# Performance work log

Hardware: AMD Instinct MI355X
Metric: run time of the kernel (lower is better)

## Reference

```python
import jax, jax.numpy as jnp
import numpy as np

LOG_STD2 = float(np.log(0.001))  # matches nn.init posterior_W_u/v fill, unused: params are random here


def _mvg_layer(x, M, u, v, eps):
    # append ones column (bias trick): [B, in] -> [B, in+1]
    x1 = jnp.concatenate([x, jnp.ones((x.shape[0], 1), x.dtype)], axis=1)
    # W = M + diag(exp(.5u)) @ eps @ diag(exp(.5v))  ==  M + row/col scaled eps
    W = M + jnp.exp(0.5 * u)[:, None] * eps * jnp.exp(0.5 * v)[None, :]
    return x1 @ W


def setup_inputs() -> dict:
    key = jax.random.key(0)
    ks = jax.random.split(key, 17)
    dims = [(2049, 4096), (4097, 4096), (4097, 4096), (4097, 2048)]
    inp = {"x": jax.random.normal(ks[0], (8192, 2048), dtype=jnp.float32)}
    ki = 1
    for i, (fin, fout) in enumerate(dims):
        inp[f"M{i}"] = jax.random.normal(ks[ki], (fin, fout), dtype=jnp.float32) * 0.001; ki += 1
        inp[f"u{i}"] = jax.random.normal(ks[ki], (fin,), dtype=jnp.float32) + LOG_STD2; ki += 1
        inp[f"v{i}"] = jax.random.normal(ks[ki], (fout,), dtype=jnp.float32) + LOG_STD2; ki += 1
        inp[f"eps{i}"] = jax.random.normal(ks[ki], (fin, fout), dtype=jnp.float32); ki += 1
    return inp


def reference(x, M0, u0, v0, eps0, M1, u1, v1, eps1, M2, u2, v2, eps2, M3, u3, v3, eps3):
    h = _mvg_layer(x, M0, u0, v0, eps0)
    h = _mvg_layer(jax.nn.relu(h), M1, u1, v1, eps1)
    h = _mvg_layer(jax.nn.relu(h), M2, u2, v2, eps2)
    h = _mvg_layer(jax.nn.relu(h), M3, u3, v3, eps3)
    return h
```

## Files before the change

kernel.cpp:

```cpp
#include <hip/hip_runtime.h>
#include <cstdint>
#include <cstddef>

typedef __bf16 bf16_t;
typedef __attribute__((ext_vector_type(8))) __bf16 bf16x8;
typedef __attribute__((ext_vector_type(4))) __bf16 bf16x4;
typedef __attribute__((ext_vector_type(4))) float floatx4;

#define SB0 __builtin_amdgcn_sched_barrier(0)
#define LGKM(N)                                          \
  do {                                                   \
    asm volatile("s_waitcnt lgkmcnt(" #N ")" ::: "memory"); \
    SB0;                                                 \
  } while (0)

__device__ __forceinline__ void cp16(const void* g, void* l) {
  __builtin_amdgcn_global_load_lds(
      (const __attribute__((address_space(1))) void*)(uintptr_t)g,
      (__attribute__((address_space(3))) void*)(uintptr_t)l, 16, 0, 0);
}

__device__ __forceinline__ void stage_half(const bf16_t* p, int K, char* dst,
                                           int tid) {
  cp16(p, dst + tid * 16);
  cp16(p + (size_t)128 * K, dst + 8192 + tid * 16);
}

__global__ void cvt_to_bf16(const float4* __restrict__ in,
                            bf16x4* __restrict__ out, int n4) {
  int i = blockIdx.x * 256 + threadIdx.x;
  if (i < n4) {
    float4 f = in[i];
    bf16x4 o;
    o[0] = (bf16_t)f.x; o[1] = (bf16_t)f.y; o[2] = (bf16_t)f.z; o[3] = (bf16_t)f.w;
    out[i] = o;
  }
}

__global__ void prep_wt(const float* __restrict__ M, const float* __restrict__ u,
                        const float* __restrict__ v, const float* __restrict__ eps,
                        bf16_t* __restrict__ Wt, int K, int N) {
  __shared__ float tile[32][33];
  const int nb = blockIdx.x * 32, kb = blockIdx.y * 32;
  const int tx = threadIdx.x, ty = threadIdx.y;
  const float sv = __expf(0.5f * v[nb + tx]);
#pragma unroll
  for (int r = 0; r < 4; ++r) {
    const int k = kb + ty + 8 * r;
    const float su = __expf(0.5f * u[k]);
    const size_t idx = (size_t)k * N + nb + tx;
    tile[ty + 8 * r][tx] = M[idx] + su * eps[idx] * sv;
  }
  __syncthreads();
#pragma unroll
  for (int r = 0; r < 4; ++r) {
    const int n = nb + ty + 8 * r;
    Wt[(size_t)n * K + kb + tx] = (bf16_t)tile[tx][ty + 8 * r];
  }
}

struct BiasArgs {
  const float* M[4];
  const float* u[4];
  const float* v[4];
  const float* e[4];
  float* b[4];
};
__global__ void prep_bias_all(BiasArgs a) {
  const int bid = blockIdx.x;
  int layer, base;
  if (bid < 16) { layer = 0; base = bid; }
  else if (bid < 32) { layer = 1; base = bid - 16; }
  else if (bid < 48) { layer = 2; base = bid - 32; }
  else { layer = 3; base = bid - 48; }
  const int K = (layer == 0) ? 2048 : 4096;
  const int N = (layer == 3) ? 2048 : 4096;
  const int n = base * 256 + threadIdx.x;
  if (n < N) {
    const size_t idx = (size_t)K * N + n;
    a.b[layer][n] = a.M[layer][idx] +
                    __expf(0.5f * a.u[layer][K]) * a.e[layer][idx] *
                        __expf(0.5f * a.v[layer][n]);
  }
}

template <int I0>
__device__ __forceinline__ void mfma_quad(const bf16x8 (&bb)[4], bf16x8 a,
                                          floatx4 (&acc)[8][4]) {
#pragma unroll
  for (int j = 0; j < 4; ++j)
    acc[I0][j] =
        __builtin_amdgcn_mfma_f32_16x16x32_bf16(bb[j], a, acc[I0][j], 0, 0, 0);
}

template <int I0>
__device__ __forceinline__ void phaseA(const char* Ab, const char* Bb,
                                       bf16x8 (&bb)[4], floatx4 (&acc)[8][4]) {
  bf16x8 af0 = *(const bf16x8*)(Ab + (I0 + 0) * 1024);
  bb[0] = *(const bf16x8*)(Bb);
  bb[1] = *(const bf16x8*)(Bb + 1024);
  bb[2] = *(const bf16x8*)(Bb + 2048);
  bb[3] = *(const bf16x8*)(Bb + 3072);
  SB0;
  bf16x8 af1 = *(const bf16x8*)(Ab + (I0 + 1) * 1024);
  SB0;
  bf16x8 af2 = *(const bf16x8*)(Ab + (I0 + 2) * 1024);
  SB0;
  bf16x8 af3 = *(const bf16x8*)(Ab + (I0 + 3) * 1024);
  __builtin_amdgcn_s_setprio(1);
  LGKM(3);
  mfma_quad<I0 + 0>(bb, af0, acc);
  LGKM(2);
  mfma_quad<I0 + 1>(bb, af1, acc);
  LGKM(1);
  mfma_quad<I0 + 2>(bb, af2, acc);
  LGKM(0);
  mfma_quad<I0 + 3>(bb, af3, acc);
  __builtin_amdgcn_s_setprio(0);
}

template <int I0>
__device__ __forceinline__ void phaseB(const char* Ab, const bf16x8 (&bb)[4],
                                       floatx4 (&acc)[8][4]) {
  bf16x8 af0 = *(const bf16x8*)(Ab + (I0 + 0) * 1024);
  SB0;
  bf16x8 af1 = *(const bf16x8*)(Ab + (I0 + 1) * 1024);
  SB0;
  bf16x8 af2 = *(const bf16x8*)(Ab + (I0 + 2) * 1024);
  SB0;
  bf16x8 af3 = *(const bf16x8*)(Ab + (I0 + 3) * 1024);
  __builtin_amdgcn_s_setprio(1);
  LGKM(3);
  mfma_quad<I0 + 0>(bb, af0, acc);
  LGKM(2);
  mfma_quad<I0 + 1>(bb, af1, acc);
  LGKM(1);
  mfma_quad<I0 + 2>(bb, af2, acc);
  LGKM(0);
  mfma_quad<I0 + 3>(bb, af3, acc);
  __builtin_amdgcn_s_setprio(0);
}

template <int CURB>
__device__ __forceinline__ void ktile(int t, int NT, int K,
                                      const bf16_t* gA, const bf16_t* gB,
                                      char* lds, int tid, int aoff0, int boff0,
                                      floatx4 (&acc)[8][4]) {
  constexpr int curO = CURB * 65536;
  constexpr int nxtO = (CURB ^ 1) * 65536;
  bf16x8 bb[4];
  const char* Ab0 = lds + curO + aoff0;
  const char* Ab1 = lds + curO + 16384 + aoff0;
  const char* Bb0 = lds + curO + 32768 + boff0;
  const char* Bb1 = lds + curO + 49152 + boff0;

  if (t + 1 < NT)
    stage_half(gA + (size_t)(t + 1) * 64 + 32, K, lds + nxtO + 16384, tid);
  phaseA<0>(Ab0, Bb0, bb, acc);
  __builtin_amdgcn_s_barrier();
  SB0;

  if (t + 1 < NT)
    stage_half(gB + (size_t)(t + 1) * 64 + 32, K, lds + nxtO + 49152, tid);
  phaseB<4>(Ab0, bb, acc);
  __builtin_amdgcn_s_barrier();
  SB0;

  if (t + 2 < NT)
    stage_half(gA + (size_t)(t + 2) * 64, K, lds + curO, tid);
  phaseA<0>(Ab1, Bb1, bb, acc);
  __builtin_amdgcn_s_barrier();
  SB0;

  if (t + 2 < NT)
    stage_half(gB + (size_t)(t + 2) * 64, K, lds + curO + 32768, tid);
  phaseB<4>(Ab1, bb, acc);
  if (t + 2 < NT) {
    asm volatile("s_waitcnt vmcnt(4)" ::: "memory");
  } else if (t + 1 < NT) {
    asm volatile("s_waitcnt vmcnt(0)" ::: "memory");
  }
  SB0;
  __builtin_amdgcn_s_barrier();
  SB0;
}

template <int EPI>
__global__ __launch_bounds__(512, 2) void gemm256(
    const bf16_t* __restrict__ A, const bf16_t* __restrict__ Bt,
    const float* __restrict__ bias, void* __restrict__ Cout, int N, int K) {
  extern __shared__ char lds[];
  const int tid = threadIdx.x;
  const int lane = tid & 63;
  const int wave = tid >> 6;
  const int wm = (wave >> 2) * 128;
  const int wn = (wave & 3) * 64;
  const int l15 = lane & 15;
  const int kqs = ((lane >> 4) ^ ((lane >> 1) & 3)) << 4;
  const int aoff0 = (wm + l15) * 64 + kqs;
  const int bofB0 = (wn + l15) * 64 + kqs;

  const int gx = gridDim.x;
  int id = blockIdx.y * gx + blockIdx.x;
  const int cpx = (gx * (int)gridDim.y) >> 3;
  id = (id & 7) * cpx + (id >> 3);
  const int bm = (id / gx) * 256;
  const int bn = (id % gx) * 256;

  const int srow = tid >> 2;
  const int ss8 = ((tid & 3) ^ ((tid >> 3) & 3)) * 8;
  const bf16_t* gA = A + (size_t)(bm + srow) * K + ss8;
  const bf16_t* gB = Bt + (size_t)(bn + srow) * K + ss8;

  const int NT = K >> 6;

  floatx4 acc[8][4] = {};

  stage_half(gA, K, lds + 0, tid);
  stage_half(gA + 32, K, lds + 16384, tid);
  stage_half(gB, K, lds + 32768, tid);
  stage_half(gB + 32, K, lds + 49152, tid);
  stage_half(gA + 64, K, lds + 65536, tid);
  stage_half(gB + 64, K, lds + 65536 + 32768, tid);
  asm volatile("s_waitcnt vmcnt(4)" ::: "memory");
  __builtin_amdgcn_s_barrier();
  SB0;

  for (int t = 0; t < NT; t += 2) {
    ktile<0>(t, NT, K, gA, gB, lds, tid, aoff0, bofB0, acc);
    ktile<1>(t + 1, NT, K, gA, gB, lds, tid, aoff0, bofB0, acc);
  }

  const int kq4 = lane >> 4;
  const int row00 = bm + wm + l15;
  const int colq = bn + wn + kq4 * 4;
  float4 b4[4];
#pragma unroll
  for (int j = 0; j < 4; ++j) b4[j] = *(const float4*)&bias[colq + j * 16];
#pragma unroll
  for (int i = 0; i < 8; ++i) {
    const size_t rbase = (size_t)(row00 + i * 16) * N;
#pragma unroll
    for (int j = 0; j < 4; ++j) {
      float x0 = acc[i][j][0] + b4[j].x;
      float x1 = acc[i][j][1] + b4[j].y;
      float x2 = acc[i][j][2] + b4[j].z;
      float x3 = acc[i][j][3] + b4[j].w;
      if (EPI == 0) {
        x0 = fmaxf(x0, 0.f);
        x1 = fmaxf(x1, 0.f);
        x2 = fmaxf(x2, 0.f);
        x3 = fmaxf(x3, 0.f);
        bf16x4 o;
        o[0] = (bf16_t)x0; o[1] = (bf16_t)x1; o[2] = (bf16_t)x2; o[3] = (bf16_t)x3;
        *(bf16x4*)((bf16_t*)Cout + rbase + colq + j * 16) = o;
      } else {
        float4 o = make_float4(x0, x1, x2, x3);
        *(float4*)((float*)Cout + rbase + colq + j * 16) = o;
      }
    }
  }
}

extern "C" void kernel_launch(void* const* d_in, const int* in_sizes, int n_in,
                              void* d_out, int out_size, void* d_ws, size_t ws_size,
                              hipStream_t stream) {
  const float* x = (const float*)d_in[0];
  const float *Mm[4], *uu[4], *vv[4], *ee[4];
  for (int i = 0; i < 4; ++i) {
    Mm[i] = (const float*)d_in[1 + 4 * i];
    uu[i] = (const float*)d_in[2 + 4 * i];
    vv[i] = (const float*)d_in[3 + 4 * i];
    ee[i] = (const float*)d_in[4 + 4 * i];
  }

  char* ws = (char*)d_ws;
  bf16_t* Wt0 = (bf16_t*)ws;
  bf16_t* Wt1 = (bf16_t*)(ws + 16777216);
  bf16_t* Wt2 = (bf16_t*)(ws + 16777216 + 33554432);
  bf16_t* Wt3 = (bf16_t*)(ws + 16777216 + 2u * 33554432);
  char* bptr = ws + 2u * 16777216 + 2u * 33554432;
  float* bias0 = (float*)(bptr);
  float* bias1 = (float*)(bptr + 16384);
  float* bias2 = (float*)(bptr + 32768);
  float* bias3 = (float*)(bptr + 49152);
  char* act = bptr + 65536;
  bf16_t* hA = (bf16_t*)act;
  bf16_t* hB = (bf16_t*)(act + 67108864);
  bf16_t* xb = (bf16_t*)d_out;

  static bool attr_set = false;
  if (!attr_set) {
    (void)hipFuncSetAttribute(reinterpret_cast<const void*>(&gemm256<0>),
                              hipFuncAttributeMaxDynamicSharedMemorySize, 131072);
    (void)hipFuncSetAttribute(reinterpret_cast<const void*>(&gemm256<1>),
                              hipFuncAttributeMaxDynamicSharedMemorySize, 131072);
    attr_set = true;
  }

  cvt_to_bf16<<<16384, 256, 0, stream>>>((const float4*)x, (bf16x4*)xb,
                                         8192 * 2048 / 4);
  prep_wt<<<dim3(4096 / 32, 2048 / 32), dim3(32, 8), 0, stream>>>(
      Mm[0], uu[0], vv[0], ee[0], Wt0, 2048, 4096);
  prep_wt<<<dim3(4096 / 32, 4096 / 32), dim3(32, 8), 0, stream>>>(
      Mm[1], uu[1], vv[1], ee[1], Wt1, 4096, 4096);
  prep_wt<<<dim3(4096 / 32, 4096 / 32), dim3(32, 8), 0, stream>>>(
      Mm[2], uu[2], vv[2], ee[2], Wt2, 4096, 4096);
  prep_wt<<<dim3(2048 / 32, 4096 / 32), dim3(32, 8), 0, stream>>>(
      Mm[3], uu[3], vv[3], ee[3], Wt3, 4096, 2048);
  BiasArgs ba;
  for (int i = 0; i < 4; ++i) {
    ba.M[i] = Mm[i]; ba.u[i] = uu[i]; ba.v[i] = vv[i]; ba.e[i] = ee[i];
  }
  ba.b[0] = bias0; ba.b[1] = bias1; ba.b[2] = bias2; ba.b[3] = bias3;
  prep_bias_all<<<56, 256, 0, stream>>>(ba);

  gemm256<0><<<dim3(16, 32), 512, 131072, stream>>>(xb, Wt0, bias0, hA, 4096, 2048);
  gemm256<0><<<dim3(16, 32), 512, 131072, stream>>>(hA, Wt1, bias1, hB, 4096, 4096);
  gemm256<0><<<dim3(16, 32), 512, 131072, stream>>>(hB, Wt2, bias2, hA, 4096, 4096);
  gemm256<1><<<dim3(8, 32), 512, 131072, stream>>>(hA, Wt3, bias3, d_out, 2048, 4096);
}
```

Baseline: 1.169 ms.

## Switch GEMM to 32x32x16 MFMA and merge prep kernels into one launch

New measurement: 1.268 ms. +8.4%, slower.

```diff
diff --git a/kernel.cpp b/kernel.cpp
--- a/kernel.cpp
+++ b/kernel.cpp
@@ -5,13 +5,13 @@
 typedef __bf16 bf16_t;
 typedef __attribute__((ext_vector_type(8))) __bf16 bf16x8;
 typedef __attribute__((ext_vector_type(4))) __bf16 bf16x4;
-typedef __attribute__((ext_vector_type(4))) float floatx4;
+typedef __attribute__((ext_vector_type(16))) float floatx16;
 
 #define SB0 __builtin_amdgcn_sched_barrier(0)
-#define LGKM(N)                                          \
-  do {                                                   \
+#define LGKM(N)                                             \
+  do {                                                      \
     asm volatile("s_waitcnt lgkmcnt(" #N ")" ::: "memory"); \
-    SB0;                                                 \
+    SB0;                                                    \
   } while (0)
 
 __device__ __forceinline__ void cp16(const void* g, void* l) {
@@ -26,23 +26,63 @@
   cp16(p + (size_t)128 * K, dst + 8192 + tid * 16);
 }
 
-__global__ void cvt_to_bf16(const float4* __restrict__ in,
-                            bf16x4* __restrict__ out, int n4) {
-  int i = blockIdx.x * 256 + threadIdx.x;
-  if (i < n4) {
-    float4 f = in[i];
+struct PrepArgs {
+  const float* x;
+  bf16_t* xb;
+  const float* M[4];
+  const float* u[4];
+  const float* v[4];
+  const float* e[4];
+  bf16_t* Wt[4];
+  float* bias[4];
+};
+
+__global__ __launch_bounds__(256) void prep_all(PrepArgs a) {
+  __shared__ float tile[32][33];
+  const int tx = threadIdx.x, ty = threadIdx.y;
+  const int tid = ty * 32 + tx;
+  int bid = blockIdx.x;
+
+  if (bid < 16384) {
+    const int i = bid * 256 + tid;
+    float4 f = ((const float4*)a.x)[i];
     bf16x4 o;
     o[0] = (bf16_t)f.x; o[1] = (bf16_t)f.y; o[2] = (bf16_t)f.z; o[3] = (bf16_t)f.w;
-    out[i] = o;
-  }
-}
-
-__global__ void prep_wt(const float* __restrict__ M, const float* __restrict__ u,
-                        const float* __restrict__ v, const float* __restrict__ eps,
-                        bf16_t* __restrict__ Wt, int K, int N) {
-  __shared__ float tile[32][33];
-  const int nb = blockIdx.x * 32, kb = blockIdx.y * 32;
-  const int tx = threadIdx.x, ty = threadIdx.y;
+    ((bf16x4*)a.xb)[i] = o;
+    return;
+  }
+  bid -= 16384;
+
+  if (bid >= 49152) {
+    const int b = bid - 49152;
+    int layer, base;
+    if (b < 16) { layer = 0; base = b; }
+    else if (b < 32) { layer = 1; base = b - 16; }
+    else if (b < 48) { layer = 2; base = b - 32; }
+    else { layer = 3; base = b - 48; }
+    const int K = (layer == 0) ? 2048 : 4096;
+    const int N = (layer == 3) ? 2048 : 4096;
+    const int n = base * 256 + tid;
+    if (n < N) {
+      const size_t idx = (size_t)K * N + n;
+      a.bias[layer][n] = a.M[layer][idx] +
+                         __expf(0.5f * a.u[layer][K]) * a.e[layer][idx] *
+                             __expf(0.5f * a.v[layer][n]);
+    }
+    return;
+  }
+
+  int layer, nbx, kby, K, N;
+  if (bid < 8192) { layer = 0; K = 2048; N = 4096; nbx = bid & 127; kby = bid >> 7; }
+  else if (bid < 24576) { layer = 1; K = 4096; N = 4096; int b = bid - 8192; nbx = b & 127; kby = b >> 7; }
+  else if (bid < 40960) { layer = 2; K = 4096; N = 4096; int b = bid - 24576; nbx = b & 127; kby = b >> 7; }
+  else { layer = 3; K = 4096; N = 2048; int b = bid - 40960; nbx = b & 63; kby = b >> 6; }
+  const float* M = a.M[layer];
+  const float* u = a.u[layer];
+  const float* v = a.v[layer];
+  const float* eps = a.e[layer];
+  bf16_t* Wt = a.Wt[layer];
+  const int nb = nbx * 32, kb = kby * 32;
   const float sv = __expf(0.5f * v[nb + tx]);
 #pragma unroll
   for (int r = 0; r < 4; ++r) {
@@ -59,122 +99,69 @@
   }
 }
 
-struct BiasArgs {
-  const float* M[4];
-  const float* u[4];
-  const float* v[4];
-  const float* e[4];
-  float* b[4];
-};
-__global__ void prep_bias_all(BiasArgs a) {
-  const int bid = blockIdx.x;
-  int layer, base;
-  if (bid < 16) { layer = 0; base = bid; }
-  else if (bid < 32) { layer = 1; base = bid - 16; }
-  else if (bid < 48) { layer = 2; base = bid - 32; }
-  else { layer = 3; base = bid - 48; }
-  const int K = (layer == 0) ? 2048 : 4096;
-  const int N = (layer == 3) ? 2048 : 4096;
-  const int n = base * 256 + threadIdx.x;
-  if (n < N) {
-    const size_t idx = (size_t)K * N + n;
-    a.b[layer][n] = a.M[layer][idx] +
-                    __expf(0.5f * a.u[layer][K]) * a.e[layer][idx] *
-                        __expf(0.5f * a.v[layer][n]);
-  }
-}
-
-template <int I0>
-__device__ __forceinline__ void mfma_quad(const bf16x8 (&bb)[4], bf16x8 a,
-                                          floatx4 (&acc)[8][4]) {
-#pragma unroll
-  for (int j = 0; j < 4; ++j)
-    acc[I0][j] =
-        __builtin_amdgcn_mfma_f32_16x16x32_bf16(bb[j], a, acc[I0][j], 0, 0, 0);
-}
-
-template <int I0>
-__device__ __forceinline__ void phaseA(const char* Ab, const char* Bb,
-                                       bf16x8 (&bb)[4], floatx4 (&acc)[8][4]) {
-  bf16x8 af0 = *(const bf16x8*)(Ab + (I0 + 0) * 1024);
-  bb[0] = *(const bf16x8*)(Bb);
-  bb[1] = *(const bf16x8*)(Bb + 1024);
-  bb[2] = *(const bf16x8*)(Bb + 2048);
-  bb[3] = *(const bf16x8*)(Bb + 3072);
-  SB0;
-  bf16x8 af1 = *(const bf16x8*)(Ab + (I0 + 1) * 1024);
-  SB0;
-  bf16x8 af2 = *(const bf16x8*)(Ab + (I0 + 2) * 1024);
-  SB0;
-  bf16x8 af3 = *(const bf16x8*)(Ab + (I0 + 3) * 1024);
+__device__ __forceinline__ void rd6(const char* HA, const char* HB, int aoff,
+                                    int boff, bf16x8 (&af)[4], bf16x8 (&bb)[2]) {
+  bb[0] = *(const bf16x8*)(HB + boff);
+  bb[1] = *(const bf16x8*)(HB + boff + 2048);
+  af[0] = *(const bf16x8*)(HA + aoff);
+  af[1] = *(const bf16x8*)(HA + aoff + 2048);
+  af[2] = *(const bf16x8*)(HA + aoff + 4096);
+  af[3] = *(const bf16x8*)(HA + aoff + 6144);
+}
+
+__device__ __forceinline__ void mf8(const bf16x8 (&af)[4], const bf16x8 (&bb)[2],
+                                    floatx16 (&acc)[4][2]) {
   __builtin_amdgcn_s_setprio(1);
-  LGKM(3);
-  mfma_quad<I0 + 0>(bb, af0, acc);
-  LGKM(2);
-  mfma_quad<I0 + 1>(bb, af1, acc);
-  LGKM(1);
-  mfma_quad<I0 + 2>(bb, af2, acc);
-  LGKM(0);
-  mfma_quad<I0 + 3>(bb, af3, acc);
+#pragma unroll
+  for (int mb = 0; mb < 4; ++mb)
+#pragma unroll
+    for (int nb = 0; nb < 2; ++nb)
+      acc[mb][nb] = __builtin_amdgcn_mfma_f32_32x32x16_bf16(
+          bb[nb], af[mb], acc[mb][nb], 0, 0, 0);
   __builtin_amdgcn_s_setprio(0);
 }
 
-template <int I0>
-__device__ __forceinline__ void phaseB(const char* Ab, const bf16x8 (&bb)[4],
-                                       floatx4 (&acc)[8][4]) {
-  bf16x8 af0 = *(const bf16x8*)(Ab + (I0 + 0) * 1024);
-  SB0;
-  bf16x8 af1 = *(const bf16x8*)(Ab + (I0 + 1) * 1024);
-  SB0;
-  bf16x8 af2 = *(const bf16x8*)(Ab + (I0 + 2) * 1024);
-  SB0;
-  bf16x8 af3 = *(const bf16x8*)(Ab + (I0 + 3) * 1024);
-  __builtin_amdgcn_s_setprio(1);
-  LGKM(3);
-  mfma_quad<I0 + 0>(bb, af0, acc);
-  LGKM(2);
-  mfma_quad<I0 + 1>(bb, af1, acc);
-  LGKM(1);
-  mfma_quad<I0 + 2>(bb, af2, acc);
-  LGKM(0);
-  mfma_quad<I0 + 3>(bb, af3, acc);
-  __builtin_amdgcn_s_setprio(0);
-}
-
 template <int CURB>
-__device__ __forceinline__ void ktile(int t, int NT, int K,
-                                      const bf16_t* gA, const bf16_t* gB,
-                                      char* lds, int tid, int aoff0, int boff0,
-                                      floatx4 (&acc)[8][4]) {
+__device__ __forceinline__ void ktile(int t, int NT, int K, const bf16_t* gA,
+                                      const bf16_t* gB, char* lds, int tid,
+                                      int aoff0, int aoff1, int boff0, int boff1,
+                                      floatx16 (&acc)[4][2]) {
   constexpr int curO = CURB * 65536;
   constexpr int nxtO = (CURB ^ 1) * 65536;
-  bf16x8 bb[4];
-  const char* Ab0 = lds + curO + aoff0;
-  const char* Ab1 = lds + curO + 16384 + aoff0;
-  const char* Bb0 = lds + curO + 32768 + boff0;
-  const char* Bb1 = lds + curO + 49152 + boff0;
-
-  if (t + 1 < NT)
+  const char* A0 = lds + curO;
+  const char* A1 = lds + curO + 16384;
+  const char* B0 = lds + curO + 32768;
+  const char* B1h = lds + curO + 49152;
+  bf16x8 afX[4], bbX[2], afY[4], bbY[2], afZ[4], bbZ[2];
+
+  if (t + 1 < NT) {
     stage_half(gA + (size_t)(t + 1) * 64 + 32, K, lds + nxtO + 16384, tid);
-  phaseA<0>(Ab0, Bb0, bb, acc);
+    stage_half(gB + (size_t)(t + 1) * 64 + 32, K, lds + nxtO + 49152, tid);
+  }
+  rd6(A0, B0, aoff0, boff0, afX, bbX);
+  SB0;
+  rd6(A0, B0, aoff1, boff1, afY, bbY);
+  SB0;
+  LGKM(6);
+  mf8(afX, bbX, acc);
+  rd6(A1, B1h, aoff0, boff0, afZ, bbZ);
+  SB0;
+  rd6(A1, B1h, aoff1, boff1, afX, bbX);
+  SB0;
+  LGKM(12);
+  mf8(afY, bbY, acc);
+  SB0;
   __builtin_amdgcn_s_barrier();
   SB0;
-
-  if (t + 1 < NT)
-    stage_half(gB + (size_t)(t + 1) * 64 + 32, K, lds + nxtO + 49152, tid);
-  phaseB<4>(Ab0, bb, acc);
-  __builtin_amdgcn_s_barrier();
-  SB0;
-
-  if (t + 2 < NT)
+  if (t + 2 < NT) {
     stage_half(gA + (size_t)(t + 2) * 64, K, lds + curO, tid);
-  phaseA<0>(Ab1, Bb1, bb, acc);
-  __builtin_amdgcn_s_barrier();
-  SB0;
-
-  if (t + 2 < NT)
     stage_half(gB + (size_t)(t + 2) * 64, K, lds + curO + 32768, tid);
-  phaseB<4>(Ab1, bb, acc);
+  }
+  LGKM(6);
+  mf8(afZ, bbZ, acc);
+  LGKM(0);
+  mf8(afX, bbX, acc);
+  SB0;
   if (t + 2 < NT) {
     asm volatile("s_waitcnt vmcnt(4)" ::: "memory");
   } else if (t + 1 < NT) {
@@ -195,10 +182,17 @@
   const int wave = tid >> 6;
   const int wm = (wave >> 2) * 128;
   const int wn = (wave & 3) * 64;
-  const int l15 = lane & 15;
-  const int kqs = ((lane >> 4) ^ ((lane >> 1) & 3)) << 4;
-  const int aoff0 = (wm + l15) * 64 + kqs;
-  const int bofB0 = (wn + l15) * 64 + kqs;
+
+  const int l31 = lane & 31;
+  const int kh = lane >> 5;
+  const int lA = wm + l31;
+  const int lB = wn + l31;
+  const int xA = (lA >> 1) & 3;
+  const int xB = (lB >> 1) & 3;
+  const int aoff0 = lA * 64 + ((kh ^ xA) << 4);
+  const int aoff1 = lA * 64 + (((2 + kh) ^ xA) << 4);
+  const int boff0 = lB * 64 + ((kh ^ xB) << 4);
+  const int boff1 = lB * 64 + (((2 + kh) ^ xB) << 4);
 
   const int gx = gridDim.x;
   int id = blockIdx.y * gx + blockIdx.x;
@@ -214,7 +208,7 @@
 
   const int NT = K >> 6;
 
-  floatx4 acc[8][4] = {};
+  floatx16 acc[4][2] = {};
 
   stage_half(gA, K, lds + 0, tid);
   stage_half(gA + 32, K, lds + 16384, tid);
@@ -227,36 +221,36 @@
   SB0;
 
   for (int t = 0; t < NT; t += 2) {
-    ktile<0>(t, NT, K, gA, gB, lds, tid, aoff0, bofB0, acc);
-    ktile<1>(t + 1, NT, K, gA, gB, lds, tid, aoff0, bofB0, acc);
-  }
-
-  const int kq4 = lane >> 4;
-  const int row00 = bm + wm + l15;
-  const int colq = bn + wn + kq4 * 4;
-  float4 b4[4];
-#pragma unroll
-  for (int j = 0; j < 4; ++j) b4[j] = *(const float4*)&bias[colq + j * 16];
-#pragma unroll
-  for (int i = 0; i < 8; ++i) {
-    const size_t rbase = (size_t)(row00 + i * 16) * N;
-#pragma unroll
-    for (int j = 0; j < 4; ++j) {
-      float x0 = acc[i][j][0] + b4[j].x;
-      float x1 = acc[i][j][1] + b4[j].y;
-      float x2 = acc[i][j][2] + b4[j].z;
-      float x3 = acc[i][j][3] + b4[j].w;
-      if (EPI == 0) {
-        x0 = fmaxf(x0, 0.f);
-        x1 = fmaxf(x1, 0.f);
-        x2 = fmaxf(x2, 0.f);
-        x3 = fmaxf(x3, 0.f);
-        bf16x4 o;
-        o[0] = (bf16_t)x0; o[1] = (bf16_t)x1; o[2] = (bf16_t)x2; o[3] = (bf16_t)x3;
-        *(bf16x4*)((bf16_t*)Cout + rbase + colq + j * 16) = o;
-      } else {
-        float4 o = make_float4(x0, x1, x2, x3);
-        *(float4*)((float*)Cout + rbase + colq + j * 16) = o;
+    ktile<0>(t, NT, K, gA, gB, lds, tid, aoff0, aoff1, boff0, boff1, acc);
+    ktile<1>(t + 1, NT, K, gA, gB, lds, tid, aoff0, aoff1, boff0, boff1, acc);
+  }
+
+  const int m0 = bm + wm + l31;
+  const int kh4 = kh * 4;
+#pragma unroll
+  for (int nb = 0; nb < 2; ++nb) {
+#pragma unroll
+    for (int q = 0; q < 4; ++q) {
+      const int col = bn + wn + nb * 32 + q * 8 + kh4;
+      const float4 b4 = *(const float4*)&bias[col];
+#pragma unroll
+      for (int mb = 0; mb < 4; ++mb) {
+        float x0 = acc[mb][nb][q * 4 + 0] + b4.x;
+        float x1 = acc[mb][nb][q * 4 + 1] + b4.y;
+        float x2 = acc[mb][nb][q * 4 + 2] + b4.z;
+        float x3 = acc[mb][nb][q * 4 + 3] + b4.w;
+        const size_t idx = (size_t)(m0 + mb * 32) * N + col;
+        if (EPI == 0) {
+          x0 = fmaxf(x0, 0.f);
+          x1 = fmaxf(x1, 0.f);
+          x2 = fmaxf(x2, 0.f);
+          x3 = fmaxf(x3, 0.f);
+          bf16x4 o;
+          o[0] = (bf16_t)x0; o[1] = (bf16_t)x1; o[2] = (bf16_t)x2; o[3] = (bf16_t)x3;
+          *(bf16x4*)((bf16_t*)Cout + idx) = o;
+        } else {
+          *(float4*)((float*)Cout + idx) = make_float4(x0, x1, x2, x3);
+        }
       }
     }
   }
@@ -298,22 +292,15 @@
     attr_set = true;
   }
 
-  cvt_to_bf16<<<16384, 256, 0, stream>>>((const float4*)x, (bf16x4*)xb,
-                                         8192 * 2048 / 4);
-  prep_wt<<<dim3(4096 / 32, 2048 / 32), dim3(32, 8), 0, stream>>>(
-      Mm[0], uu[0], vv[0], ee[0], Wt0, 2048, 4096);
-  prep_wt<<<dim3(4096 / 32, 4096 / 32), dim3(32, 8), 0, stream>>>(
-      Mm[1], uu[1], vv[1], ee[1], Wt1, 4096, 4096);
-  prep_wt<<<dim3(4096 / 32, 4096 / 32), dim3(32, 8), 0, stream>>>(
-      Mm[2], uu[2], vv[2], ee[2], Wt2, 4096, 4096);
-  prep_wt<<<dim3(2048 / 32, 4096 / 32), dim3(32, 8), 0, stream>>>(
-      Mm[3], uu[3], vv[3], ee[3], Wt3, 4096, 2048);
-  BiasArgs ba;
+  PrepArgs pa;
+  pa.x = x;
+  pa.xb = xb;
   for (int i = 0; i < 4; ++i) {
-    ba.M[i] = Mm[i]; ba.u[i] = uu[i]; ba.v[i] = vv[i]; ba.e[i] = ee[i];
-  }
-  ba.b[0] = bias0; ba.b[1] = bias1; ba.b[2] = bias2; ba.b[3] = bias3;
-  prep_bias_all<<<56, 256, 0, stream>>>(ba);
+    pa.M[i] = Mm[i]; pa.u[i] = uu[i]; pa.v[i] = vv[i]; pa.e[i] = ee[i];
+  }
+  pa.Wt[0] = Wt0; pa.Wt[1] = Wt1; pa.Wt[2] = Wt2; pa.Wt[3] = Wt3;
+  pa.bias[0] = bias0; pa.bias[1] = bias1; pa.bias[2] = bias2; pa.bias[3] = bias3;
+  prep_all<<<16384 + 49152 + 56, dim3(32, 8), 0, stream>>>(pa);
 
   gemm256<0><<<dim3(16, 32), 512, 131072, stream>>>(xb, Wt0, bias0, hA, 4096, 2048);
   gemm256<0><<<dim3(16, 32), 512, 131072, stream>>>(hA, Wt1, bias1, hB, 4096, 4096);
```
